# Performance work log

Measured on AMD Instinct MI355X. Metric: run time of the kernel, lower is better.

Reference implementation:

```python
import jax, jax.numpy as jnp
import numpy as np


def setup_inputs() -> dict:
    key = jax.random.key(0)
    k1, k2 = jax.random.split(key)
    n, m, p, d = 32, 16, 1024, 512
    task = jax.random.normal(k1, (n, m, p), dtype=jnp.float32)
    feat = jax.random.normal(k2, (n, p, d), dtype=jnp.float32)
    return {"task": task, "feat": feat}


def reference(task, feat):
    # Original: mean_m( feat[n,1,p,d] * task[n,m,p,1] ) over dim m.
    # Since feat is independent of m, this equals feat * mean_m(task),
    # avoiding the O(n*m*p*d) intermediate while computing identical math.
    task_mean = jnp.mean(task, axis=1)          # [n, p]
    return feat * task_mean[..., None]           # [n, p, d]
```

## Files before the change

kernel.cpp:

```cpp
#include <hip/hip_runtime.h>


#define N_DIM 32
#define M_DIM 16
#define P_DIM 1024
#define D_DIM 512

__global__ __launch_bounds__(128) void MAP_20023137534634_kernel(
    const float* __restrict__ task,
    const float* __restrict__ feat,
    float* __restrict__ out)
{
    const int np = blockIdx.x;
    const int n  = np >> 10;
    const int p  = np & (P_DIM - 1);

    const float* tptr = task + ((size_t)n * M_DIM) * P_DIM + p;
    float s = 0.0f;
#pragma unroll
    for (int m = 0; m < M_DIM; ++m) {
        s += tptr[(size_t)m * P_DIM];
    }
    const float mean = s * (1.0f / (float)M_DIM);

    const size_t base = (size_t)np * D_DIM;
    const float4* f4 = (const float4*)(feat + base);
    float4*       o4 = (float4*)(out + base);

    float4 v = f4[threadIdx.x];
    v.x *= mean; v.y *= mean; v.z *= mean; v.w *= mean;
    o4[threadIdx.x] = v;
}

extern "C" void kernel_launch(void* const* d_in, const int* in_sizes, int n_in,
                              void* d_out, int out_size, void* d_ws, size_t ws_size,
                              hipStream_t stream) {
    const float* task = (const float*)d_in[0];
    const float* feat = (const float*)d_in[1];
    float* out = (float*)d_out;

    dim3 grid(N_DIM * P_DIM);
    dim3 block(128);
    MAP_20023137534634_kernel<<<grid, block, 0, stream>>>(task, feat, out);
}
```

Baseline: 118.6 us.

## Split mean reduction and broadcast scale into two separate kernels

Moves the per-(n,p) mean over m into its own kernel that writes a workspace buffer. A second flat elementwise kernel then scales feat by the stored mean. The old fused kernel had every block do 16 strided scalar task loads before its float4 work. Splitting removes that serialised reduction from the bandwidth-bound scale pass, at the cost of an extra launch and a small mean buffer round-trip.

```diff
diff --git a/kernel.cpp b/kernel.cpp
--- a/kernel.cpp
+++ b/kernel.cpp
@@ -5,31 +5,35 @@
 #define M_DIM 16
 #define P_DIM 1024
 #define D_DIM 512
+#define NP    (N_DIM * P_DIM)
+#define TOTAL4 (NP * (D_DIM / 4))
 
-__global__ __launch_bounds__(128) void MAP_20023137534634_kernel(
+__global__ __launch_bounds__(256) void mean_kernel(
     const float* __restrict__ task,
-    const float* __restrict__ feat,
-    float* __restrict__ out)
+    float* __restrict__ mean)
 {
-    const int np = blockIdx.x;
-    const int n  = np >> 10;
-    const int p  = np & (P_DIM - 1);
-
-    const float* tptr = task + ((size_t)n * M_DIM) * P_DIM + p;
+    const int i = blockIdx.x * 256 + threadIdx.x;
+    const int n = i >> 10;
+    const int p = i & (P_DIM - 1);
+    const float* t = task + (size_t)n * M_DIM * P_DIM + p;
     float s = 0.0f;
 #pragma unroll
     for (int m = 0; m < M_DIM; ++m) {
-        s += tptr[(size_t)m * P_DIM];
+        s += t[(size_t)m * P_DIM];
     }
-    const float mean = s * (1.0f / (float)M_DIM);
+    mean[i] = s * (1.0f / (float)M_DIM);
+}
 
-    const size_t base = (size_t)np * D_DIM;
-    const float4* f4 = (const float4*)(feat + base);
-    float4*       o4 = (float4*)(out + base);
-
-    float4 v = f4[threadIdx.x];
-    v.x *= mean; v.y *= mean; v.z *= mean; v.w *= mean;
-    o4[threadIdx.x] = v;
+__global__ __launch_bounds__(256) void scale_kernel(
+    const float* __restrict__ feat,
+    const float* __restrict__ mean,
+    float* __restrict__ out)
+{
+    const int idx4 = blockIdx.x * 256 + threadIdx.x;
+    const float m = mean[idx4 >> 7];
+    float4 v = ((const float4*)feat)[idx4];
+    v.x *= m; v.y *= m; v.z *= m; v.w *= m;
+    ((float4*)out)[idx4] = v;
 }
 
 extern "C" void kernel_launch(void* const* d_in, const int* in_sizes, int n_in,
@@ -37,9 +41,9 @@
                               hipStream_t stream) {
     const float* task = (const float*)d_in[0];
     const float* feat = (const float*)d_in[1];
-    float* out = (float*)d_out;
+    float* out  = (float*)d_out;
+    float* mean = (float*)d_ws;
 
-    dim3 grid(N_DIM * P_DIM);
-    dim3 block(128);
-    MAP_20023137534634_kernel<<<grid, block, 0, stream>>>(task, feat, out);
+    mean_kernel<<<dim3(NP / 256), dim3(256), 0, stream>>>(task, mean);
+    scale_kernel<<<dim3(TOTAL4 / 256), dim3(256), 0, stream>>>(feat, mean, out);
 }
```

After: 116.4 us, median of 2. Within noise of the previous version (-1.8%).

## Process 32 rows per block with coalesced task loads and nontemporal feat streaming

Applied to the files above, without the earlier changes.

Each block now handles 32 consecutive p rows with 512 threads. The task slice is loaded cooperatively into shared memory with coalesced reads, reduced over m, and broadcast. The feat multiply uses several float4 nontemporal loads and stores per thread. This is meant to replace the strided per-block task reads and the many tiny blocks with fewer, larger ones that stream memory better, at the cost of two barriers per block.

```diff
diff --git a/kernel.cpp b/kernel.cpp
--- a/kernel.cpp
+++ b/kernel.cpp
@@ -5,31 +5,56 @@
 #define M_DIM 16
 #define P_DIM 1024
 #define D_DIM 512
+#define ROWS_PER_BLK 32
+#define F4_PER_ROW   (D_DIM / 4)
+#define F4_PER_BLK   (ROWS_PER_BLK * F4_PER_ROW)
+#define BLK_THREADS  512
+#define F4_PER_THR   (F4_PER_BLK / BLK_THREADS)
+#define GRID_BLKS    (N_DIM * P_DIM / ROWS_PER_BLK)
 
-__global__ __launch_bounds__(128) void MAP_20023137534634_kernel(
+typedef float vfloat4 __attribute__((ext_vector_type(4)));
+
+__global__ __launch_bounds__(BLK_THREADS) void fused_kernel(
     const float* __restrict__ task,
     const float* __restrict__ feat,
     float* __restrict__ out)
 {
-    const int np = blockIdx.x;
-    const int n  = np >> 10;
-    const int p  = np & (P_DIM - 1);
+    __shared__ float lds_v[M_DIM][ROWS_PER_BLK];
+    __shared__ float lds_mean[ROWS_PER_BLK];
 
-    const float* tptr = task + ((size_t)n * M_DIM) * P_DIM + p;
-    float s = 0.0f;
+    const int b  = blockIdx.x;
+    const int n  = b >> 5;
+    const int p0 = (b & 31) * ROWS_PER_BLK;
+    const int t  = threadIdx.x;
+
+    {
+        const int m  = t >> 5;
+        const int po = t & 31;
+        lds_v[m][po] = task[((size_t)n * M_DIM + m) * P_DIM + p0 + po];
+    }
+    __syncthreads();
+    if (t < ROWS_PER_BLK) {
+        float s = 0.0f;
 #pragma unroll
-    for (int m = 0; m < M_DIM; ++m) {
-        s += tptr[(size_t)m * P_DIM];
+        for (int m = 0; m < M_DIM; ++m) s += lds_v[m][t];
+        lds_mean[t] = s * (1.0f / (float)M_DIM);
     }
-    const float mean = s * (1.0f / (float)M_DIM);
+    __syncthreads();
 
-    const size_t base = (size_t)np * D_DIM;
-    const float4* f4 = (const float4*)(feat + base);
-    float4*       o4 = (float4*)(out + base);
+    float mr[F4_PER_THR];
+#pragma unroll
+    for (int i = 0; i < F4_PER_THR; ++i) mr[i] = lds_mean[4 * i + (t >> 7)];
 
-    float4 v = f4[threadIdx.x];
-    v.x *= mean; v.y *= mean; v.z *= mean; v.w *= mean;
-    o4[threadIdx.x] = v;
+    const size_t base4 = (size_t)b * F4_PER_BLK;
+    const vfloat4* f4 = (const vfloat4*)feat + base4;
+    vfloat4*       o4 = (vfloat4*)out + base4;
+#pragma unroll
+    for (int i = 0; i < F4_PER_THR; ++i) {
+        const int idx = i * BLK_THREADS + t;
+        vfloat4 v = __builtin_nontemporal_load(f4 + idx);
+        v *= mr[i];
+        __builtin_nontemporal_store(v, o4 + idx);
+    }
 }
 
 extern "C" void kernel_launch(void* const* d_in, const int* in_sizes, int n_in,
@@ -39,7 +64,5 @@
     const float* feat = (const float*)d_in[1];
     float* out = (float*)d_out;
 
-    dim3 grid(N_DIM * P_DIM);
-    dim3 block(128);
-    MAP_20023137534634_kernel<<<grid, block, 0, stream>>>(task, feat, out);
+    fused_kernel<<<dim3(GRID_BLKS), dim3(BLK_THREADS), 0, stream>>>(task, feat, out);
 }
```

New measurement: 120.4 us. No clear change (+1.5%).
